# Kernel optimization log

Measured on AMD Instinct MI355X. Metric: run time of the kernel, lower is better.

Reference implementation:

```python
import jax, jax.numpy as jnp
import numpy as np

P = 16; RES = 224; D = 768; L = 12; H = 12; OUT = 512
NP1 = NP2 = RES // P          # 14x14 patches
NTOK = NP1 * NP2 + 1          # 197 tokens (cls + patches)
STD = 5.0                     # gaussian_std for naclip
EPS = 1e-5


def _ln(x, w, b):
    x32 = x.astype(jnp.float32)
    m = x32.mean(-1, keepdims=True)
    v = ((x32 - m) ** 2).mean(-1, keepdims=True)
    return (((x32 - m) * jax.lax.rsqrt(v + EPS)) * w + b).astype(x.dtype)


def _quick_gelu(x):
    return x * jax.nn.sigmoid(1.702 * x)


def _gaussian_addition():
    # VisionTransformer.gaussian_window + get_attention_addition, done analytically:
    # addition[i*NP2+j, k*NP2+l] = window[k-i+NP1-1, l-j+NP2-1]
    w1, w2 = 2 * NP1 - 1, 2 * NP2 - 1
    c = 1.0 / (STD * np.sqrt(2.0))
    k1 = (-(w1 - 1) / 2.0 + np.arange(w1)) * c
    k2 = (-(w2 - 1) / 2.0 + np.arange(w2)) * c
    window = np.exp(-(k1[:, None] ** 2 + k2[None, :] ** 2))
    r = np.arange(NP1)[None, :] - np.arange(NP1)[:, None] + (NP1 - 1)  # [i,k]
    cc = np.arange(NP2)[None, :] - np.arange(NP2)[:, None] + (NP2 - 1)  # [j,l]
    A = window[r[:, None, :, None], cc[None, :, None, :]]  # (NP1,NP2,NP1,NP2)
    A = A.reshape(NP1 * NP2, NP1 * NP2)
    full = np.zeros((NTOK, NTOK), dtype=np.float32)
    full[1:, 1:] = A  # zero row/col for cls token
    return jnp.asarray(full)


def _mha_vanilla(x, wi, bi, wo, bo):
    B, N, _ = x.shape
    hd = D // H
    qkv = x @ wi.T + bi                      # [B,N,3D]
    q, k, v = jnp.split(qkv, 3, axis=-1)
    q = q.reshape(B, N, H, hd); k = k.reshape(B, N, H, hd); v = v.reshape(B, N, H, hd)
    a = jnp.einsum('bqhd,bkhd->bhqk', q, k) * (hd ** -0.5)
    a = jax.nn.softmax(a, axis=-1)
    o = jnp.einsum('bhqk,bkhd->bqhd', a, v).reshape(B, N, D)
    return o @ wo.T + bo


def _mha_naclip(x, wi, bi, wo, bo, addition):
    B, N, _ = x.shape
    hd = D // H
    qkv = x @ wi.T + bi
    _, k, v = jnp.split(qkv, 3, axis=-1)
    k = k.reshape(B, N, H, hd); v = v.reshape(B, N, H, hd)
    a = jnp.einsum('bqhd,bkhd->bhqk', k, k) * (hd ** -0.5) + addition[None, None]
    a = jax.nn.softmax(a, axis=-1)
    o = jnp.einsum('bhqk,bkhd->bqhd', a, v).reshape(B, N, D)
    return o @ wo.T + bo


def _mlp(x, fw, fb, pw, pb):
    return _quick_gelu(x @ fw.T + fb) @ pw.T + pb


def setup_inputs() -> dict:
    key = jax.random.key(0)
    ks = jax.random.split(key, 16)
    s = D ** -0.5
    rn = lambda k, shape, sc=0.02: jax.random.normal(k, shape, jnp.float32) * sc
    return {
        'x': jax.random.normal(ks[0], (32, 3, RES, RES), jnp.float32),
        'conv1_w': rn(ks[1], (D, 3, P, P)),
        'class_embedding': rn(ks[2], (D,), s),
        'pos_embedding': rn(ks[3], (NTOK, D), s),
        'ln_pre_w': jnp.ones((D,)), 'ln_pre_b': jnp.zeros((D,)),
        'in_proj_w': rn(ks[4], (L, 3 * D, D)), 'in_proj_b': rn(ks[5], (L, 3 * D)),
        'out_proj_w': rn(ks[6], (L, D, D)), 'out_proj_b': rn(ks[7], (L, D)),
        'ln1_w': jnp.ones((L, D)), 'ln1_b': jnp.zeros((L, D)),
        'ln2_w': jnp.ones((L, D)), 'ln2_b': jnp.zeros((L, D)),
        'fc_w': rn(ks[8], (L, 4 * D, D)), 'fc_b': rn(ks[9], (L, 4 * D)),
        'cproj_w': rn(ks[10], (L, D, 4 * D)), 'cproj_b': rn(ks[11], (L, D)),
        'ln_post_w': jnp.ones((D,)), 'ln_post_b': jnp.zeros((D,)),
        'proj': rn(ks[12], (D, OUT), s),
    }


def reference(x, conv1_w, class_embedding, pos_embedding, ln_pre_w, ln_pre_b,
              in_proj_w, in_proj_b, out_proj_w, out_proj_b, ln1_w, ln1_b,
              ln2_w, ln2_b, fc_w, fc_b, cproj_w, cproj_b, ln_post_w, ln_post_b, proj):
    B = x.shape[0]
    # patch embed
    h = jax.lax.conv_general_dilated(x, conv1_w, (P, P), 'VALID',
                                     dimension_numbers=('NCHW', 'OIHW', 'NCHW'))
    h = h.reshape(B, D, NP1 * NP2).transpose(0, 2, 1)           # [B,196,D]
    cls = jnp.broadcast_to(class_embedding, (B, 1, D))
    h = jnp.concatenate([cls, h], axis=1) + pos_embedding        # [B,197,D]
    h = _ln(h, ln_pre_w, ln_pre_b)
    addition = _gaussian_addition()
    # first L-1 blocks: vanilla attention
    for i in range(L - 1):
        h = h + _mha_vanilla(_ln(h, ln1_w[i], ln1_b[i]), in_proj_w[i], in_proj_b[i],
                             out_proj_w[i], out_proj_b[i])
        h = h + _mlp(_ln(h, ln2_w[i], ln2_b[i]), fc_w[i], fc_b[i], cproj_w[i], cproj_b[i])
    # last block: naclip key-key attention with gaussian addition (arch='vanilla')
    i = L - 1
    reduced = _mha_naclip(_ln(h, ln1_w[i], ln1_b[i]), in_proj_w[i], in_proj_b[i],
                          out_proj_w[i], out_proj_b[i], addition)
    final = h + reduced
    final = final + _mlp(_ln(final, ln2_w[i], ln2_b[i]), fc_w[i], fc_b[i], cproj_w[i], cproj_b[i])
    return _ln(final, ln_post_w, ln_post_b) @ proj               # [B,197,OUT]
```

## Files before the change

kernel.cpp:

```cpp
#include <hip/hip_runtime.h>
#include <hip/hip_bf16.h>
#include <math.h>

#define BATCH 32
#define NTOK  197
#define NPATCH 196
#define DMODEL 768
#define NLAYER 12
#define NHEAD 12
#define HDIM  64
#define ROWS  (BATCH*NTOK)
#define CROWS (BATCH*NPATCH)
#define DFF   3072
#define DQKV  2304
#define DOUT  512
#define NBH   (BATCH*NHEAD)

#define WS_H    ((size_t)0)
#define WS_QKV  ((size_t)ROWS*DMODEL)
#define WS_SC   (WS_QKV + (size_t)ROWS*DQKV)
#define WS_TB   (WS_SC + (size_t)NBH*NTOK*NTOK)
#define WS_WB   (WS_TB + (size_t)ROWS*DMODEL/2)
#define WS_PTS  (WS_WB + (size_t)DFF*DMODEL/2)
#define WS_ADD  (WS_PTS + (size_t)DOUT*DMODEL/2)

typedef unsigned short ushort_t;
typedef __attribute__((ext_vector_type(8))) short bf16x8;
typedef __attribute__((ext_vector_type(4))) float f32x4;

__device__ inline ushort_t bf16rn(float x) {
    uint32_t u = __builtin_bit_cast(uint32_t, x);
    uint32_t r = (u + 0x7FFFu + ((u >> 16) & 1u)) >> 16;
    return (ushort_t)r;
}


__global__ void im2col_bf16_k(const float* __restrict__ x, ushort_t* __restrict__ out) {
    int idx = blockIdx.x * 256 + threadIdx.x;
    if (idx >= CROWS * DMODEL / 4) return;
    int r  = idx / (DMODEL / 4);
    int k4 = (idx - r * (DMODEL / 4)) * 4;
    int b = r / NPATCH, p = r - b * NPATCH;
    int py = p / 14, px = p - py * 14;
    int c = k4 >> 8, rem = k4 & 255, i = rem >> 4, j = rem & 15;
    const float* xp = x + (((size_t)(b * 3 + c) * 224) + py * 16 + i) * 224 + px * 16 + j;
    float4 v = *(const float4*)xp;
    ushort4 hv = {bf16rn(v.x), bf16rn(v.y), bf16rn(v.z), bf16rn(v.w)};
    *(ushort4*)(out + (size_t)r * DMODEL + k4) = hv;
}

__global__ void cvt_w_k(const float* __restrict__ W, ushort_t* __restrict__ out, int NK) {
    int idx = (blockIdx.x * 256 + threadIdx.x) * 4;
    if (idx >= NK) return;
    float4 v = *(const float4*)(W + idx);
    ushort4 hv = {bf16rn(v.x), bf16rn(v.y), bf16rn(v.z), bf16rn(v.w)};
    *(ushort4*)(out + idx) = hv;
}

__global__ void cvt_pT_k(const float* __restrict__ proj, ushort_t* __restrict__ out) {
    int idx = blockIdx.x * 256 + threadIdx.x;
    if (idx >= DOUT * DMODEL) return;
    int n = idx / DMODEL, k = idx - n * DMODEL;
    out[(size_t)n * DMODEL + k] = bf16rn(proj[(size_t)k * DOUT + n]);
}

__global__ void embed_k(const float* __restrict__ conv, const float* __restrict__ cls,
                        const float* __restrict__ pos, float* __restrict__ h) {
    int idx = blockIdx.x * 256 + threadIdx.x;
    if (idx >= ROWS * DMODEL) return;
    int r = idx / DMODEL, d = idx - r * DMODEL;
    int b = r / NTOK, tok = r - b * NTOK;
    float v = (tok == 0) ? cls[d] : conv[((size_t)(b * NPATCH + tok - 1)) * DMODEL + d];
    h[idx] = v + pos[(size_t)tok * DMODEL + d];
}

__global__ void gauss_k(float* __restrict__ add) {
    int idx = blockIdx.x * 256 + threadIdx.x;
    if (idx >= NTOK * NTOK) return;
    int i = idx / NTOK, j = idx - i * NTOK;
    float v = 0.f;
    if (i > 0 && j > 0) {
        int p = i - 1, q = j - 1;
        int di = q / 14 - p / 14;
        int dj = q % 14 - p % 14;
        v = expf(-(float)(di * di + dj * dj) * 0.02f);
    }
    add[idx] = v;
}

__global__ __launch_bounds__(256) void ln768_k(const float* __restrict__ in, float* __restrict__ out,
                                               const float* __restrict__ w, const float* __restrict__ b) {
    int row = blockIdx.x, tid = threadIdx.x;
    const float* x = in + (size_t)row * DMODEL;
    float v0 = x[tid], v1 = x[tid + 256], v2 = x[tid + 512];
    float s = v0 + v1 + v2;
    float s2 = v0 * v0 + v1 * v1 + v2 * v2;
    for (int o = 32; o > 0; o >>= 1) { s += __shfl_down(s, o); s2 += __shfl_down(s2, o); }
    __shared__ float red[8];
    int wid = tid >> 6;
    if ((tid & 63) == 0) { red[wid] = s; red[4 + wid] = s2; }
    __syncthreads();
    s  = red[0] + red[1] + red[2] + red[3];
    s2 = red[4] + red[5] + red[6] + red[7];
    float mean = s * (1.0f / 768.0f);
    float var  = s2 * (1.0f / 768.0f) - mean * mean;
    float rinv = rsqrtf(var + 1e-5f);
    float* o_ = out + (size_t)row * DMODEL;
    o_[tid]       = (v0 - mean) * rinv * w[tid]       + b[tid];
    o_[tid + 256] = (v1 - mean) * rinv * w[tid + 256] + b[tid + 256];
    o_[tid + 512] = (v2 - mean) * rinv * w[tid + 512] + b[tid + 512];
}

__global__ __launch_bounds__(256) void ln768_bf16_k(const float* __restrict__ in, ushort_t* __restrict__ out,
                                                    const float* __restrict__ w, const float* __restrict__ b) {
    int row = blockIdx.x, tid = threadIdx.x;
    const float* x = in + (size_t)row * DMODEL;
    float v0 = x[tid], v1 = x[tid + 256], v2 = x[tid + 512];
    float s = v0 + v1 + v2;
    float s2 = v0 * v0 + v1 * v1 + v2 * v2;
    for (int o = 32; o > 0; o >>= 1) { s += __shfl_down(s, o); s2 += __shfl_down(s2, o); }
    __shared__ float red[8];
    int wid = tid >> 6;
    if ((tid & 63) == 0) { red[wid] = s; red[4 + wid] = s2; }
    __syncthreads();
    s  = red[0] + red[1] + red[2] + red[3];
    s2 = red[4] + red[5] + red[6] + red[7];
    float mean = s * (1.0f / 768.0f);
    float var  = s2 * (1.0f / 768.0f) - mean * mean;
    float rinv = rsqrtf(var + 1e-5f);
    ushort_t* o_ = out + (size_t)row * DMODEL;
    o_[tid]       = bf16rn((v0 - mean) * rinv * w[tid]       + b[tid]);
    o_[tid + 256] = bf16rn((v1 - mean) * rinv * w[tid + 256] + b[tid + 256]);
    o_[tid + 512] = bf16rn((v2 - mean) * rinv * w[tid + 512] + b[tid + 512]);
}

__global__ __launch_bounds__(256) void gemm_mfma_k(
    const ushort_t* __restrict__ A, const ushort_t* __restrict__ W,
    const float* __restrict__ bias, float* __restrict__ C, ushort_t* __restrict__ OS,
    int M, int N, int K, int mode)
{
    __shared__ ushort_t As[128][32];
    __shared__ ushort_t Bs[128][32];
    int tid = threadIdx.x;
    int lane = tid & 63;
    int wave = tid >> 6;
    int wm = wave >> 1, wn = wave & 1;
    int m0 = blockIdx.y * 128, n0 = blockIdx.x * 128;

    int klen = K / gridDim.z;
    int kbeg = blockIdx.z * klen;

    f32x4 acc[4][4];
    #pragma unroll
    for (int i = 0; i < 4; ++i)
        #pragma unroll
        for (int j = 0; j < 4; ++j)
            acc[i][j] = (f32x4){0.f, 0.f, 0.f, 0.f};

    int srow = tid >> 2;
    int skq  = (((tid & 3) ^ ((tid >> 3) & 3)) * 8);
    int ar0 = m0 + srow;      if (ar0 > M - 1) ar0 = M - 1;
    int ar1 = m0 + srow + 64; if (ar1 > M - 1) ar1 = M - 1;
    const ushort_t* Ap0 = A + (size_t)ar0 * K + kbeg + skq;
    const ushort_t* Ap1 = A + (size_t)ar1 * K + kbeg + skq;
    const ushort_t* Wp0 = W + (size_t)(n0 + srow) * K + kbeg + skq;
    const ushort_t* Wp1 = W + (size_t)(n0 + srow + 64) * K + kbeg + skq;
    char* ldsA0 = (char*)&As[0][0] + tid * 16;
    char* ldsA1 = ldsA0 + 4096;
    char* ldsB0 = (char*)&Bs[0][0] + tid * 16;
    char* ldsB1 = ldsB0 + 4096;

    int fr = lane & 15, fq = lane >> 4;
    int rsl = (fq ^ ((fr >> 1) & 3)) * 8;

    for (int k0 = 0; k0 < klen; k0 += 32) {
        __builtin_amdgcn_global_load_lds((const __attribute__((address_space(1))) void*)(Ap0 + k0),
                                         (__attribute__((address_space(3))) void*)ldsA0, 16, 0, 0);
        __builtin_amdgcn_global_load_lds((const __attribute__((address_space(1))) void*)(Ap1 + k0),
                                         (__attribute__((address_space(3))) void*)ldsA1, 16, 0, 0);
        __builtin_amdgcn_global_load_lds((const __attribute__((address_space(1))) void*)(Wp0 + k0),
                                         (__attribute__((address_space(3))) void*)ldsB0, 16, 0, 0);
        __builtin_amdgcn_global_load_lds((const __attribute__((address_space(1))) void*)(Wp1 + k0),
                                         (__attribute__((address_space(3))) void*)ldsB1, 16, 0, 0);
        __syncthreads();

        bf16x8 a[4], b[4];
        #pragma unroll
        for (int fm = 0; fm < 4; ++fm)
            a[fm] = *(const bf16x8*)&As[wm * 64 + fm * 16 + fr][rsl];
        #pragma unroll
        for (int fn = 0; fn < 4; ++fn)
            b[fn] = *(const bf16x8*)&Bs[wn * 64 + fn * 16 + fr][rsl];
        #pragma unroll
        for (int fm = 0; fm < 4; ++fm)
            #pragma unroll
            for (int fn = 0; fn < 4; ++fn)
                acc[fm][fn] = __builtin_amdgcn_mfma_f32_16x16x32_bf16(a[fm], b[fn], acc[fm][fn], 0, 0, 0);
        __syncthreads();
    }

    #pragma unroll
    for (int fn = 0; fn < 4; ++fn) {
        int ccol = n0 + wn * 64 + fn * 16 + fr;
        float bv = bias ? bias[ccol] : 0.f;
        if (mode == 3 && blockIdx.z != 0) bv = 0.f;
        #pragma unroll
        for (int fm = 0; fm < 4; ++fm) {
            int crow0 = m0 + wm * 64 + fm * 16 + fq * 4;
            #pragma unroll
            for (int j = 0; j < 4; ++j) {
                int row = crow0 + j;
                if (row < M) {
                    float v = acc[fm][fn][j] + bv;
                    if (mode == 0) {
                        C[(size_t)row * N + ccol] = v;
                    } else if (mode == 2) {
                        C[(size_t)row * N + ccol] += v;
                    } else if (mode == 3) {
                        atomicAdd(&C[(size_t)row * N + ccol], v);
                    } else {
                        v = v / (1.0f + expf(-1.702f * v));
                        OS[(size_t)row * N + ccol] = bf16rn(v);
                    }
                }
            }
        }
    }
}

__global__ __launch_bounds__(256) void attn_fused_k(
    const float* __restrict__ qkv, ushort_t* __restrict__ out,
    const float* __restrict__ addition, int qoff)
{
    __shared__ ushort_t Ks[208][72];
    __shared__ ushort_t Vt[64][232];
    __shared__ ushort_t Pb[4][16][40];
    int tid = threadIdx.x;
    int bh = blockIdx.x;
    int b = bh / NHEAD, hh = bh - b * NHEAD;
    const float* base = qkv + (size_t)b * NTOK * DQKV + hh * HDIM;

    {
        int tt = tid >> 4, dq = tid & 15;
        #pragma unroll
        for (int pass = 0; pass < 13; ++pass) {
            int t = pass * 16 + tt;
            float4 kv = {0, 0, 0, 0}, vv = {0, 0, 0, 0};
            if (t < NTOK) {
                kv = *(const float4*)(base + (size_t)t * DQKV + DMODEL + dq * 4);
                vv = *(const float4*)(base + (size_t)t * DQKV + 2 * DMODEL + dq * 4);
            }
            ushort4 kh = {bf16rn(kv.x), bf16rn(kv.y), bf16rn(kv.z), bf16rn(kv.w)};
            *(ushort4*)&Ks[t][dq * 4] = kh;
            Vt[dq * 4 + 0][t] = bf16rn(vv.x);
            Vt[dq * 4 + 1][t] = bf16rn(vv.y);
            Vt[dq * 4 + 2][t] = bf16rn(vv.z);
            Vt[dq * 4 + 3][t] = bf16rn(vv.w);
        }
        for (int z = tid; z < 64 * 24; z += 256) Vt[z / 24][208 + z % 24] = 0;
    }
    __syncthreads();

    int lane = tid & 63, wave = tid >> 6;
    int fr = lane & 15, fq = lane >> 4;

    for (int qt = wave; qt < 13; qt += 4) {
        int i0 = qt * 16;
        int qrow = i0 + fr; if (qrow > NTOK - 1) qrow = NTOK - 1;
        const float* qp = base + (size_t)qrow * DQKV + qoff + fq * 8;
        float4 qa = *(const float4*)(qp);
        float4 qb = *(const float4*)(qp + 4);
        float4 qc = *(const float4*)(qp + 32);
        float4 qd = *(const float4*)(qp + 36);
        bf16x8 q0, q1;
        q0[0] = (short)bf16rn(qa.x); q0[1] = (short)bf16rn(qa.y);
        q0[2] = (short)bf16rn(qa.z); q0[3] = (short)bf16rn(qa.w);
        q0[4] = (short)bf16rn(qb.x); q0[5] = (short)bf16rn(qb.y);
        q0[6] = (short)bf16rn(qb.z); q0[7] = (short)bf16rn(qb.w);
        q1[0] = (short)bf16rn(qc.x); q1[1] = (short)bf16rn(qc.y);
        q1[2] = (short)bf16rn(qc.z); q1[3] = (short)bf16rn(qc.w);
        q1[4] = (short)bf16rn(qd.x); q1[5] = (short)bf16rn(qd.y);
        q1[6] = (short)bf16rn(qd.z); q1[7] = (short)bf16rn(qd.w);

        f32x4 s[13];
        #pragma unroll
        for (int jt = 0; jt < 13; ++jt) {
            bf16x8 k0 = *(const bf16x8*)&Ks[jt * 16 + fr][fq * 8];
            bf16x8 k1 = *(const bf16x8*)&Ks[jt * 16 + fr][32 + fq * 8];
            f32x4 a = {0.f, 0.f, 0.f, 0.f};
            a = __builtin_amdgcn_mfma_f32_16x16x32_bf16(q0, k0, a, 0, 0, 0);
            a = __builtin_amdgcn_mfma_f32_16x16x32_bf16(q1, k1, a, 0, 0, 0);
            s[jt] = a;
        }

        int irow[4];
        #pragma unroll
        for (int jj = 0; jj < 4; ++jj) {
            int ir = i0 + fq * 4 + jj;
            irow[jj] = (ir < NTOK) ? ir : (NTOK - 1);
        }
        float m[4] = {-1e30f, -1e30f, -1e30f, -1e30f};
        #pragma unroll
        for (int jt = 0; jt < 13; ++jt) {
            int jcol = jt * 16 + fr;
            #pragma unroll
            for (int jj = 0; jj < 4; ++jj) {
                float v = s[jt][jj] * 0.125f;
                if (addition) v += addition[irow[jj] * NTOK + (jcol < NTOK ? jcol : 0)];
                if (jcol >= NTOK) v = -1e30f;
                s[jt][jj] = v;
                m[jj] = fmaxf(m[jj], v);
            }
        }
        #pragma unroll
        for (int jj = 0; jj < 4; ++jj) {
            m[jj] = fmaxf(m[jj], __shfl_xor(m[jj], 1));
            m[jj] = fmaxf(m[jj], __shfl_xor(m[jj], 2));
            m[jj] = fmaxf(m[jj], __shfl_xor(m[jj], 4));
            m[jj] = fmaxf(m[jj], __shfl_xor(m[jj], 8));
        }
        float sum[4] = {0.f, 0.f, 0.f, 0.f};
        #pragma unroll
        for (int jt = 0; jt < 13; ++jt)
            #pragma unroll
            for (int jj = 0; jj < 4; ++jj) {
                float e = __expf(s[jt][jj] - m[jj]);
                s[jt][jj] = e;
                sum[jj] += e;
            }
        #pragma unroll
        for (int jj = 0; jj < 4; ++jj) {
            sum[jj] += __shfl_xor(sum[jj], 1);
            sum[jj] += __shfl_xor(sum[jj], 2);
            sum[jj] += __shfl_xor(sum[jj], 4);
            sum[jj] += __shfl_xor(sum[jj], 8);
        }
        float inv[4];
        #pragma unroll
        for (int jj = 0; jj < 4; ++jj) inv[jj] = 1.0f / sum[jj];

        f32x4 o4[4];
        #pragma unroll
        for (int dt = 0; dt < 4; ++dt) o4[dt] = (f32x4){0.f, 0.f, 0.f, 0.f};
        for (int st = 0; st < 7; ++st) {
            #pragma unroll
            for (int half = 0; half < 2; ++half) {
                int jt = st * 2 + half;
                #pragma unroll
                for (int jj = 0; jj < 4; ++jj) {
                    ushort_t pv = 0;
                    if (jt < 13) pv = bf16rn(s[jt][jj] * inv[jj]);
                    Pb[wave][fq * 4 + jj][half * 16 + fr] = pv;
                }
            }
            asm volatile("s_waitcnt lgkmcnt(0)" ::: "memory");
            bf16x8 pa = *(const bf16x8*)&Pb[wave][fr][fq * 8];
            #pragma unroll
            for (int dt = 0; dt < 4; ++dt) {
                bf16x8 vf = *(const bf16x8*)&Vt[dt * 16 + fr][st * 32 + fq * 8];
                o4[dt] = __builtin_amdgcn_mfma_f32_16x16x32_bf16(pa, vf, o4[dt], 0, 0, 0);
            }
        }

        #pragma unroll
        for (int jj = 0; jj < 4; ++jj) {
            int ir = i0 + fq * 4 + jj;
            if (ir < NTOK) {
                ushort_t* op = out + ((size_t)(b * NTOK + ir)) * DMODEL + hh * HDIM + fr;
                #pragma unroll
                for (int dt = 0; dt < 4; ++dt)
                    op[dt * 16] = bf16rn(o4[dt][jj]);
            }
        }
    }
}

extern "C" void kernel_launch(void* const* d_in, const int* in_sizes, int n_in,
                              void* d_out, int out_size, void* d_ws, size_t ws_size,
                              hipStream_t stream) {
    const float* x        = (const float*)d_in[0];
    const float* conv1_w  = (const float*)d_in[1];
    const float* cls      = (const float*)d_in[2];
    const float* pos      = (const float*)d_in[3];
    const float* ln_pre_w = (const float*)d_in[4];
    const float* ln_pre_b = (const float*)d_in[5];
    const float* in_proj_w  = (const float*)d_in[6];
    const float* in_proj_b  = (const float*)d_in[7];
    const float* out_proj_w = (const float*)d_in[8];
    const float* out_proj_b = (const float*)d_in[9];
    const float* ln1_w = (const float*)d_in[10];
    const float* ln1_b = (const float*)d_in[11];
    const float* ln2_w = (const float*)d_in[12];
    const float* ln2_b = (const float*)d_in[13];
    const float* fc_w  = (const float*)d_in[14];
    const float* fc_b  = (const float*)d_in[15];
    const float* cproj_w = (const float*)d_in[16];
    const float* cproj_b = (const float*)d_in[17];
    const float* ln_post_w = (const float*)d_in[18];
    const float* ln_post_b = (const float*)d_in[19];
    const float* proj = (const float*)d_in[20];
    float* out = (float*)d_out;

    float* ws   = (float*)d_ws;
    float* h    = ws + WS_H;
    float* qkv  = ws + WS_QKV;
    ushort_t* gb   = (ushort_t*)(ws + WS_SC);
    ushort_t* tb   = (ushort_t*)(ws + WS_TB);
    ushort_t* wbuf = (ushort_t*)(ws + WS_WB);
    ushort_t* pTs  = (ushort_t*)(ws + WS_PTS);
    float* add  = ws + WS_ADD;

    im2col_bf16_k<<<(CROWS * DMODEL / 4 + 255) / 256, 256, 0, stream>>>(x, tb);
    cvt_w_k<<<(DMODEL * DMODEL / 4 + 255) / 256, 256, 0, stream>>>(conv1_w, wbuf, DMODEL * DMODEL);
    gemm_mfma_k<<<dim3(DMODEL / 128, (CROWS + 127) / 128), 256, 0, stream>>>(
        tb, wbuf, nullptr, qkv, nullptr, CROWS, DMODEL, DMODEL, 0);
    embed_k<<<(ROWS * DMODEL + 255) / 256, 256, 0, stream>>>(qkv, cls, pos, h);
    ln768_k<<<ROWS, 256, 0, stream>>>(h, h, ln_pre_w, ln_pre_b);
    gauss_k<<<(NTOK * NTOK + 255) / 256, 256, 0, stream>>>(add);
    cvt_pT_k<<<(DOUT * DMODEL + 255) / 256, 256, 0, stream>>>(proj, pTs);

    const int GY = (ROWS + 127) / 128;
    for (int l = 0; l < NLAYER; ++l) {
        ln768_bf16_k<<<ROWS, 256, 0, stream>>>(h, tb, ln1_w + l * DMODEL, ln1_b + l * DMODEL);
        cvt_w_k<<<(DQKV * DMODEL / 4 + 255) / 256, 256, 0, stream>>>(
            in_proj_w + (size_t)l * DQKV * DMODEL, wbuf, DQKV * DMODEL);
        gemm_mfma_k<<<dim3(DQKV / 128, GY), 256, 0, stream>>>(
            tb, wbuf, in_proj_b + (size_t)l * DQKV, qkv, nullptr, ROWS, DQKV, DMODEL, 0);
        bool nac = (l == NLAYER - 1);
        attn_fused_k<<<NBH, 256, 0, stream>>>(qkv, tb, nac ? add : nullptr, nac ? DMODEL : 0);
        cvt_w_k<<<(DMODEL * DMODEL / 4 + 255) / 256, 256, 0, stream>>>(
            out_proj_w + (size_t)l * DMODEL * DMODEL, wbuf, DMODEL * DMODEL);
        gemm_mfma_k<<<dim3(DMODEL / 128, GY, 2), 256, 0, stream>>>(
            tb, wbuf, out_proj_b + (size_t)l * DMODEL, h, nullptr, ROWS, DMODEL, DMODEL, 3);
        ln768_bf16_k<<<ROWS, 256, 0, stream>>>(h, tb, ln2_w + l * DMODEL, ln2_b + l * DMODEL);
        cvt_w_k<<<(DFF * DMODEL / 4 + 255) / 256, 256, 0, stream>>>(
            fc_w + (size_t)l * DFF * DMODEL, wbuf, DFF * DMODEL);
        gemm_mfma_k<<<dim3(DFF / 128, GY), 256, 0, stream>>>(
            tb, wbuf, fc_b + (size_t)l * DFF, nullptr, gb, ROWS, DFF, DMODEL, 1);
        cvt_w_k<<<(DMODEL * DFF / 4 + 255) / 256, 256, 0, stream>>>(
            cproj_w + (size_t)l * DMODEL * DFF, wbuf, DMODEL * DFF);
        gemm_mfma_k<<<dim3(DMODEL / 128, GY, 2), 256, 0, stream>>>(
            gb, wbuf, cproj_b + (size_t)l * DMODEL, h, nullptr, ROWS, DMODEL, DFF, 3);
    }

    ln768_bf16_k<<<ROWS, 256, 0, stream>>>(h, tb, ln_post_w, ln_post_b);
    gemm_mfma_k<<<dim3(DOUT / 128, GY), 256, 0, stream>>>(
        tb, pTs, nullptr, out, nullptr, ROWS, DOUT, DMODEL, 0);
}
```

Baseline: 3.867 ms.

## Double-buffer GEMM LDS loads, store QKV as bf16, batch per-layer weight conversion

The GEMM kernel now uses two LDS buffers and prefetches the next K tile with global_load_lds while the current tile runs on the MFMAs. Raw s_waitcnt and s_barrier replace the __syncthreads pair. The QKV projection writes bf16 instead of fp32, so attention reads half the bytes and skips its own conversion. The four per-layer weight conversions are merged into one launch writing a contiguous weight buffer. The costs are a doubled LDS footprint per block, which may lower occupancy, and an extra bf16 rounding of QKV that was already applied inside attention before.

```diff
diff --git a/kernel.cpp b/kernel.cpp
--- a/kernel.cpp
+++ b/kernel.cpp
@@ -16,12 +16,18 @@
 #define DOUT  512
 #define NBH   (BATCH*NHEAD)
 
+#define WOFF_IN   ((size_t)0)
+#define WOFF_OUT  ((size_t)(DQKV*DMODEL))
+#define WOFF_FC   (WOFF_OUT + (size_t)(DMODEL*DMODEL))
+#define WOFF_CP   (WOFF_FC + (size_t)(DFF*DMODEL))
+#define WTOT      (WOFF_CP + (size_t)(DMODEL*DFF))
+
 #define WS_H    ((size_t)0)
-#define WS_QKV  ((size_t)ROWS*DMODEL)
-#define WS_SC   (WS_QKV + (size_t)ROWS*DQKV)
-#define WS_TB   (WS_SC + (size_t)NBH*NTOK*NTOK)
-#define WS_WB   (WS_TB + (size_t)ROWS*DMODEL/2)
-#define WS_PTS  (WS_WB + (size_t)DFF*DMODEL/2)
+#define WS_QKVB (WS_H + (size_t)ROWS*DMODEL)
+#define WS_GB   (WS_QKVB + (size_t)ROWS*DQKV/2)
+#define WS_TB   (WS_GB + (size_t)ROWS*DFF/2)
+#define WS_WL   (WS_TB + (size_t)ROWS*DMODEL/2)
+#define WS_PTS  (WS_WL + WTOT/2)
 #define WS_ADD  (WS_PTS + (size_t)DOUT*DMODEL/2)
 
 typedef unsigned short ushort_t;
@@ -33,6 +39,10 @@
     uint32_t r = (u + 0x7FFFu + ((u >> 16) & 1u)) >> 16;
     return (ushort_t)r;
 }
+
+#define GLL(src, dst) __builtin_amdgcn_global_load_lds( \
+    (const __attribute__((address_space(1))) void*)(src), \
+    (__attribute__((address_space(3))) void*)(dst), 16, 0, 0)
 
 
 __global__ void im2col_bf16_k(const float* __restrict__ x, ushort_t* __restrict__ out) {
@@ -55,6 +65,21 @@
     float4 v = *(const float4*)(W + idx);
     ushort4 hv = {bf16rn(v.x), bf16rn(v.y), bf16rn(v.z), bf16rn(v.w)};
     *(ushort4*)(out + idx) = hv;
+}
+
+__global__ void cvt_layer_k(const float* __restrict__ inW, const float* __restrict__ outW,
+                            const float* __restrict__ fcW, const float* __restrict__ cpW,
+                            ushort_t* __restrict__ wl) {
+    size_t idx = ((size_t)blockIdx.x * 256 + threadIdx.x) * 4;
+    if (idx >= WTOT) return;
+    const float* src; size_t off;
+    if (idx < WOFF_OUT)      { src = inW;  off = idx; }
+    else if (idx < WOFF_FC)  { src = outW; off = idx - WOFF_OUT; }
+    else if (idx < WOFF_CP)  { src = fcW;  off = idx - WOFF_FC; }
+    else                     { src = cpW;  off = idx - WOFF_CP; }
+    float4 v = *(const float4*)(src + off);
+    ushort4 hv = {bf16rn(v.x), bf16rn(v.y), bf16rn(v.z), bf16rn(v.w)};
+    *(ushort4*)(wl + idx) = hv;
 }
 
 __global__ void cvt_pT_k(const float* __restrict__ proj, ushort_t* __restrict__ out) {
@@ -139,8 +164,8 @@
     const float* __restrict__ bias, float* __restrict__ C, ushort_t* __restrict__ OS,
     int M, int N, int K, int mode)
 {
-    __shared__ ushort_t As[128][32];
-    __shared__ ushort_t Bs[128][32];
+    __shared__ ushort_t As[2][128][32];
+    __shared__ ushort_t Bs[2][128][32];
     int tid = threadIdx.x;
     int lane = tid & 63;
     int wave = tid >> 6;
@@ -149,6 +174,7 @@
 
     int klen = K / gridDim.z;
     int kbeg = blockIdx.z * klen;
+    int nt = klen / 32;
 
     f32x4 acc[4][4];
     #pragma unroll
@@ -165,38 +191,43 @@
     const ushort_t* Ap1 = A + (size_t)ar1 * K + kbeg + skq;
     const ushort_t* Wp0 = W + (size_t)(n0 + srow) * K + kbeg + skq;
     const ushort_t* Wp1 = W + (size_t)(n0 + srow + 64) * K + kbeg + skq;
-    char* ldsA0 = (char*)&As[0][0] + tid * 16;
-    char* ldsA1 = ldsA0 + 4096;
-    char* ldsB0 = (char*)&Bs[0][0] + tid * 16;
-    char* ldsB1 = ldsB0 + 4096;
+    char* ldsA = (char*)As + tid * 16;
+    char* ldsB = (char*)Bs + tid * 16;
 
     int fr = lane & 15, fq = lane >> 4;
     int rsl = (fq ^ ((fr >> 1) & 3)) * 8;
 
-    for (int k0 = 0; k0 < klen; k0 += 32) {
-        __builtin_amdgcn_global_load_lds((const __attribute__((address_space(1))) void*)(Ap0 + k0),
-                                         (__attribute__((address_space(3))) void*)ldsA0, 16, 0, 0);
-        __builtin_amdgcn_global_load_lds((const __attribute__((address_space(1))) void*)(Ap1 + k0),
-                                         (__attribute__((address_space(3))) void*)ldsA1, 16, 0, 0);
-        __builtin_amdgcn_global_load_lds((const __attribute__((address_space(1))) void*)(Wp0 + k0),
-                                         (__attribute__((address_space(3))) void*)ldsB0, 16, 0, 0);
-        __builtin_amdgcn_global_load_lds((const __attribute__((address_space(1))) void*)(Wp1 + k0),
-                                         (__attribute__((address_space(3))) void*)ldsB1, 16, 0, 0);
-        __syncthreads();
-
+    GLL(Ap0, ldsA);
+    GLL(Ap1, ldsA + 4096);
+    GLL(Wp0, ldsB);
+    GLL(Wp1, ldsB + 4096);
+
+    for (int t = 0; t < nt; ++t) {
+        int cur = t & 1;
+        if (t + 1 < nt) {
+            int nx = cur ^ 1;
+            size_t ko = (size_t)(t + 1) * 32;
+            GLL(Ap0 + ko, ldsA + nx * 8192);
+            GLL(Ap1 + ko, ldsA + nx * 8192 + 4096);
+            GLL(Wp0 + ko, ldsB + nx * 8192);
+            GLL(Wp1 + ko, ldsB + nx * 8192 + 4096);
+            asm volatile("s_waitcnt vmcnt(4)\n\ts_barrier" ::: "memory");
+        } else {
+            asm volatile("s_waitcnt vmcnt(0)\n\ts_barrier" ::: "memory");
+        }
         bf16x8 a[4], b[4];
         #pragma unroll
         for (int fm = 0; fm < 4; ++fm)
-            a[fm] = *(const bf16x8*)&As[wm * 64 + fm * 16 + fr][rsl];
+            a[fm] = *(const bf16x8*)&As[cur][wm * 64 + fm * 16 + fr][rsl];
         #pragma unroll
         for (int fn = 0; fn < 4; ++fn)
-            b[fn] = *(const bf16x8*)&Bs[wn * 64 + fn * 16 + fr][rsl];
+            b[fn] = *(const bf16x8*)&Bs[cur][wn * 64 + fn * 16 + fr][rsl];
         #pragma unroll
         for (int fm = 0; fm < 4; ++fm)
             #pragma unroll
             for (int fn = 0; fn < 4; ++fn)
                 acc[fm][fn] = __builtin_amdgcn_mfma_f32_16x16x32_bf16(a[fm], b[fn], acc[fm][fn], 0, 0, 0);
-        __syncthreads();
+        asm volatile("s_barrier" ::: "memory");
     }
 
     #pragma unroll
@@ -214,10 +245,10 @@
                     float v = acc[fm][fn][j] + bv;
                     if (mode == 0) {
                         C[(size_t)row * N + ccol] = v;
-                    } else if (mode == 2) {
-                        C[(size_t)row * N + ccol] += v;
                     } else if (mode == 3) {
                         atomicAdd(&C[(size_t)row * N + ccol], v);
+                    } else if (mode == 4) {
+                        OS[(size_t)row * N + ccol] = bf16rn(v);
                     } else {
                         v = v / (1.0f + expf(-1.702f * v));
                         OS[(size_t)row * N + ccol] = bf16rn(v);
@@ -229,7 +260,7 @@
 }
 
 __global__ __launch_bounds__(256) void attn_fused_k(
-    const float* __restrict__ qkv, ushort_t* __restrict__ out,
+    const ushort_t* __restrict__ qkvb, ushort_t* __restrict__ out,
     const float* __restrict__ addition, int qoff)
 {
     __shared__ ushort_t Ks[208][72];
@@ -238,24 +269,23 @@
     int tid = threadIdx.x;
     int bh = blockIdx.x;
     int b = bh / NHEAD, hh = bh - b * NHEAD;
-    const float* base = qkv + (size_t)b * NTOK * DQKV + hh * HDIM;
+    const ushort_t* base = qkvb + (size_t)b * NTOK * DQKV + hh * HDIM;
 
     {
         int tt = tid >> 4, dq = tid & 15;
         #pragma unroll
         for (int pass = 0; pass < 13; ++pass) {
             int t = pass * 16 + tt;
-            float4 kv = {0, 0, 0, 0}, vv = {0, 0, 0, 0};
+            ushort4 kv = {0, 0, 0, 0}, vv = {0, 0, 0, 0};
             if (t < NTOK) {
-                kv = *(const float4*)(base + (size_t)t * DQKV + DMODEL + dq * 4);
-                vv = *(const float4*)(base + (size_t)t * DQKV + 2 * DMODEL + dq * 4);
-            }
-            ushort4 kh = {bf16rn(kv.x), bf16rn(kv.y), bf16rn(kv.z), bf16rn(kv.w)};
-            *(ushort4*)&Ks[t][dq * 4] = kh;
-            Vt[dq * 4 + 0][t] = bf16rn(vv.x);
-            Vt[dq * 4 + 1][t] = bf16rn(vv.y);
-            Vt[dq * 4 + 2][t] = bf16rn(vv.z);
-            Vt[dq * 4 + 3][t] = bf16rn(vv.w);
+                kv = *(const ushort4*)(base + (size_t)t * DQKV + DMODEL + dq * 4);
+                vv = *(const ushort4*)(base + (size_t)t * DQKV + 2 * DMODEL + dq * 4);
+            }
+            *(ushort4*)&Ks[t][dq * 4] = kv;
+            Vt[dq * 4 + 0][t] = vv.x;
+            Vt[dq * 4 + 1][t] = vv.y;
+            Vt[dq * 4 + 2][t] = vv.z;
+            Vt[dq * 4 + 3][t] = vv.w;
         }
         for (int z = tid; z < 64 * 24; z += 256) Vt[z / 24][208 + z % 24] = 0;
     }
@@ -267,20 +297,9 @@
     for (int qt = wave; qt < 13; qt += 4) {
         int i0 = qt * 16;
         int qrow = i0 + fr; if (qrow > NTOK - 1) qrow = NTOK - 1;
-        const float* qp = base + (size_t)qrow * DQKV + qoff + fq * 8;
-        float4 qa = *(const float4*)(qp);
-        float4 qb = *(const float4*)(qp + 4);
-        float4 qc = *(const float4*)(qp + 32);
-        float4 qd = *(const float4*)(qp + 36);
-        bf16x8 q0, q1;
-        q0[0] = (short)bf16rn(qa.x); q0[1] = (short)bf16rn(qa.y);
-        q0[2] = (short)bf16rn(qa.z); q0[3] = (short)bf16rn(qa.w);
-        q0[4] = (short)bf16rn(qb.x); q0[5] = (short)bf16rn(qb.y);
-        q0[6] = (short)bf16rn(qb.z); q0[7] = (short)bf16rn(qb.w);
-        q1[0] = (short)bf16rn(qc.x); q1[1] = (short)bf16rn(qc.y);
-        q1[2] = (short)bf16rn(qc.z); q1[3] = (short)bf16rn(qc.w);
-        q1[4] = (short)bf16rn(qd.x); q1[5] = (short)bf16rn(qd.y);
-        q1[6] = (short)bf16rn(qd.z); q1[7] = (short)bf16rn(qd.w);
+        const ushort_t* qp = base + (size_t)qrow * DQKV + qoff + fq * 8;
+        bf16x8 q0 = *(const bf16x8*)qp;
+        bf16x8 q1 = *(const bf16x8*)(qp + 32);
 
         f32x4 s[13];
         #pragma unroll
@@ -403,44 +422,40 @@
 
     float* ws   = (float*)d_ws;
     float* h    = ws + WS_H;
-    float* qkv  = ws + WS_QKV;
-    ushort_t* gb   = (ushort_t*)(ws + WS_SC);
+    float* ctmp = ws + WS_QKVB;
+    ushort_t* qkvb = (ushort_t*)(ws + WS_QKVB);
+    ushort_t* gb   = (ushort_t*)(ws + WS_GB);
     ushort_t* tb   = (ushort_t*)(ws + WS_TB);
-    ushort_t* wbuf = (ushort_t*)(ws + WS_WB);
+    ushort_t* wl   = (ushort_t*)(ws + WS_WL);
     ushort_t* pTs  = (ushort_t*)(ws + WS_PTS);
     float* add  = ws + WS_ADD;
 
     im2col_bf16_k<<<(CROWS * DMODEL / 4 + 255) / 256, 256, 0, stream>>>(x, tb);
-    cvt_w_k<<<(DMODEL * DMODEL / 4 + 255) / 256, 256, 0, stream>>>(conv1_w, wbuf, DMODEL * DMODEL);
+    cvt_w_k<<<(DMODEL * DMODEL / 4 + 255) / 256, 256, 0, stream>>>(conv1_w, wl, DMODEL * DMODEL);
     gemm_mfma_k<<<dim3(DMODEL / 128, (CROWS + 127) / 128), 256, 0, stream>>>(
-        tb, wbuf, nullptr, qkv, nullptr, CROWS, DMODEL, DMODEL, 0);
-    embed_k<<<(ROWS * DMODEL + 255) / 256, 256, 0, stream>>>(qkv, cls, pos, h);
+        tb, wl, nullptr, ctmp, nullptr, CROWS, DMODEL, DMODEL, 0);
+    embed_k<<<(ROWS * DMODEL + 255) / 256, 256, 0, stream>>>(ctmp, cls, pos, h);
     ln768_k<<<ROWS, 256, 0, stream>>>(h, h, ln_pre_w, ln_pre_b);
     gauss_k<<<(NTOK * NTOK + 255) / 256, 256, 0, stream>>>(add);
     cvt_pT_k<<<(DOUT * DMODEL + 255) / 256, 256, 0, stream>>>(proj, pTs);
 
     const int GY = (ROWS + 127) / 128;
     for (int l = 0; l < NLAYER; ++l) {
+        cvt_layer_k<<<(int)(WTOT / 4 / 256), 256, 0, stream>>>(
+            in_proj_w + (size_t)l * DQKV * DMODEL, out_proj_w + (size_t)l * DMODEL * DMODEL,
+            fc_w + (size_t)l * DFF * DMODEL, cproj_w + (size_t)l * DMODEL * DFF, wl);
         ln768_bf16_k<<<ROWS, 256, 0, stream>>>(h, tb, ln1_w + l * DMODEL, ln1_b + l * DMODEL);
-        cvt_w_k<<<(DQKV * DMODEL / 4 + 255) / 256, 256, 0, stream>>>(
-            in_proj_w + (size_t)l * DQKV * DMODEL, wbuf, DQKV * DMODEL);
         gemm_mfma_k<<<dim3(DQKV / 128, GY), 256, 0, stream>>>(
-            tb, wbuf, in_proj_b + (size_t)l * DQKV, qkv, nullptr, ROWS, DQKV, DMODEL, 0);
+            tb, wl + WOFF_IN, in_proj_b + (size_t)l * DQKV, nullptr, qkvb, ROWS, DQKV, DMODEL, 4);
         bool nac = (l == NLAYER - 1);
-        attn_fused_k<<<NBH, 256, 0, stream>>>(qkv, tb, nac ? add : nullptr, nac ? DMODEL : 0);
-        cvt_w_k<<<(DMODEL * DMODEL / 4 + 255) / 256, 256, 0, stream>>>(
-            out_proj_w + (size_t)l * DMODEL * DMODEL, wbuf, DMODEL * DMODEL);
+        attn_fused_k<<<NBH, 256, 0, stream>>>(qkvb, tb, nac ? add : nullptr, nac ? DMODEL : 0);
         gemm_mfma_k<<<dim3(DMODEL / 128, GY, 2), 256, 0, stream>>>(
-            tb, wbuf, out_proj_b + (size_t)l * DMODEL, h, nullptr, ROWS, DMODEL, DMODEL, 3);
+            tb, wl + WOFF_OUT, out_proj_b + (size_t)l * DMODEL, h, nullptr, ROWS, DMODEL, DMODEL, 3);
         ln768_bf16_k<<<ROWS, 256, 0, stream>>>(h, tb, ln2_w + l * DMODEL, ln2_b + l * DMODEL);
-        cvt_w_k<<<(DFF * DMODEL / 4 + 255) / 256, 256, 0, stream>>>(
-            fc_w + (size_t)l * DFF * DMODEL, wbuf, DFF * DMODEL);
         gemm_mfma_k<<<dim3(DFF / 128, GY), 256, 0, stream>>>(
-            tb, wbuf, fc_b + (size_t)l * DFF, nullptr, gb, ROWS, DFF, DMODEL, 1);
-        cvt_w_k<<<(DMODEL * DFF / 4 + 255) / 256, 256, 0, stream>>>(
-            cproj_w + (size_t)l * DMODEL * DFF, wbuf, DMODEL * DFF);
+            tb, wl + WOFF_FC, fc_b + (size_t)l * DFF, nullptr, gb, ROWS, DFF, DMODEL, 1);
         gemm_mfma_k<<<dim3(DMODEL / 128, GY, 2), 256, 0, stream>>>(
-            gb, wbuf, cproj_b + (size_t)l * DMODEL, h, nullptr, ROWS, DMODEL, DFF, 3);
+            gb, wl + WOFF_CP, cproj_b + (size_t)l * DMODEL, h, nullptr, ROWS, DMODEL, DFF, 3);
     }
 
     ln768_bf16_k<<<ROWS, 256, 0, stream>>>(h, tb, ln_post_w, ln_post_b);
```

Result: faster. 3.540 ms (-8.5%).
